# Optimization experiments

Measured on AMD Instinct MI355X. Metric: run time of the kernel, lower is better.

The kernel has to match this reference:

```python
import jax, jax.numpy as jnp
import numpy as np
from jax import lax

B, H, W = 8, 96, 160
CF = 64        # feature channels (= input_channels//2 = out_channels)
OC = 64        # out channels
K = 3          # kernel
G = 8          # deform (offset) groups
PAD, DIL = 1, 1


def conv3x3(x, w, b):
    y = lax.conv_general_dilated(x, w, (1, 1), ((PAD, PAD), (PAD, PAD)),
                                 dimension_numbers=('NCHW', 'OIHW', 'NCHW'))
    return y + b[None, :, None, None]


def lrelu(x):
    return jnp.where(x >= 0, x, 0.1 * x)


def deform_conv2d(x, offset, mask, w, b):
    # x: (B, Cin, H, W); offset: (B, 2*G*K*K, H, W) in (y, x) per tap; mask: (B, G*K*K, H, W)
    Bq, Cin, Hq, Wq = x.shape
    OCq = w.shape[0]
    off = offset.reshape(Bq, G, K, K, 2, Hq, Wq)
    dy, dx = off[:, :, :, :, 0], off[:, :, :, :, 1]        # (B,G,K,K,H,W)
    ky = jnp.arange(K, dtype=x.dtype).reshape(1, 1, K, 1, 1, 1)
    kx = jnp.arange(K, dtype=x.dtype).reshape(1, 1, 1, K, 1, 1)
    hy = jnp.arange(Hq, dtype=x.dtype).reshape(1, 1, 1, 1, Hq, 1)
    wx = jnp.arange(Wq, dtype=x.dtype).reshape(1, 1, 1, 1, 1, Wq)
    ys = dy + hy - PAD + ky * DIL                          # sampling rows
    xs = dx + wx - PAAD if False else dx + wx - PAD + kx * DIL  # sampling cols
    xg = x.reshape(Bq, G, Cin // G, Hq, Wq)

    def sample(img, ysg, xsg):
        # img: (Cg,H,W); ysg/xsg: (K,K,H,W) -> (Cg,K,K,H,W) bilinear with zero padding
        y0 = jnp.floor(ysg)
        x0 = jnp.floor(xsg)
        wy1 = ysg - y0
        wx1 = xsg - x0
        wy0 = 1.0 - wy1
        wx0 = 1.0 - wx1

        def gather(yi, xi):
            valid = ((yi >= 0) & (yi < Hq) & (xi >= 0) & (xi < Wq)).astype(img.dtype)
            yc = jnp.clip(yi, 0, Hq - 1).astype(jnp.int32)
            xc = jnp.clip(xi, 0, Wq - 1).astype(jnp.int32)
            return img[:, yc, xc] * valid[None]

        return (gather(y0, x0) * (wy0 * wx0)[None]
                + gather(y0, x0 + 1) * (wy0 * wx1)[None]
                + gather(y0 + 1, x0) * (wy1 * wx0)[None]
                + gather(y0 + 1, x0 + 1) * (wy1 * wx1)[None])

    sampled = jax.vmap(jax.vmap(sample))(xg, ys, xs)       # (B,G,Cg,K,K,H,W)
    sampled = sampled * mask.reshape(Bq, G, 1, K, K, Hq, Wq)
    wg = w.reshape(OCq, G, Cin // G, K, K)
    return jnp.einsum('bgcijhw,ogcij->bohw', sampled, wg) + b[None, :, None, None]


def setup_inputs() -> dict:
    key = jax.random.key(0)
    ks = jax.random.split(key, 12)
    cin0 = OC * 3 + 4  # 196

    def u(k, shape, fan_in):
        s = 1.0 / np.sqrt(fan_in)
        return jax.random.uniform(k, shape, jnp.float32, -s, s)

    inp = {
        'current_feature_warped': jax.random.normal(ks[0], (B, CF, H, W), jnp.float32),
        'feat_prop': jax.random.normal(ks[1], (B, CF, H, W), jnp.float32),
        'feat_prev': jax.random.normal(ks[2], (B, CF, H, W), jnp.float32),
        'flow1': jax.random.normal(ks[3], (B, 2, H, W), jnp.float32),
        'flow2': jax.random.normal(ks[4], (B, 2, H, W), jnp.float32),
        'w1': u(ks[5], (OC, cin0, 3, 3), cin0 * 9), 'b1': jnp.zeros((OC,), jnp.float32),
        'w2': u(ks[6], (OC, OC, 3, 3), OC * 9), 'b2': jnp.zeros((OC,), jnp.float32),
        'w3': u(ks[7], (OC, OC, 3, 3), OC * 9), 'b3': jnp.zeros((OC,), jnp.float32),
        'w4': u(ks[8], (K * K * 3 * G, OC, 3, 3), OC * 9), 'b4': jnp.zeros((K * K * 3 * G,), jnp.float32),
        'weight': u(ks[9], (OC, CF, 3, 3), 128 * 9),  # init_weights uses n = input_channels*k*k = 128*9
        'bias': jnp.zeros((OC,), jnp.float32),
    }
    return inp

# remove the accidental typo guard (keeps module exec-clean)
PAAD = PAD


def reference(current_feature_warped, feat_prop, feat_prev, flow1, flow2,
              w1, b1, w2, b2, w3, b3, w4, b4, weight, bias):
    cat = jnp.concatenate([current_feature_warped, feat_prop, feat_prev, flow1, flow2], axis=1)
    o = lrelu(conv3x3(cat, w1, b1))
    o = lrelu(conv3x3(o, w2, b2))
    o = lrelu(conv3x3(o, w3, b3))
    o = conv3x3(o, w4, b4)                                  # (B, 3*G*K*K, H, W)
    offset1, offset2, mask = jnp.split(o, 3, axis=1)        # each (B, G*K*K, H, W)
    rep = offset1.shape[1] // 2                             # G*K*K/2 = 36
    offset1 = offset1 + jnp.tile(flow1[:, ::-1], (1, rep, 1, 1))
    offset2 = offset2 + jnp.tile(flow2[:, ::-1], (1, rep, 1, 1))
    offset = jnp.concatenate([offset1, offset2], axis=1)    # (B, 2*G*K*K, H, W)
    mask = jax.nn.sigmoid(mask)
    return deform_conv2d(current_feature_warped, offset, mask, weight, bias)
```

## Files before the change

### kernel.cpp

```cpp
#include <hip/hip_runtime.h>
#include <hip/hip_bf16.h>
#include <math.h>

typedef __attribute__((ext_vector_type(8))) short short8;
typedef __attribute__((ext_vector_type(4))) float f32x4;

constexpr int B_ = 8, H_ = 96, W_ = 160;
constexpr int HW_ = H_ * W_;
constexpr int NPIX = B_ * HW_;

__device__ __forceinline__ unsigned short f2bf(float f) {
    unsigned int u = __builtin_bit_cast(unsigned int, f);
    u += 0x7FFFu + ((u >> 16) & 1u);
    return (unsigned short)(u >> 16);
}
__device__ __forceinline__ float bf2f(unsigned short s) {
    unsigned int u = ((unsigned int)s) << 16;
    return __builtin_bit_cast(float, u);
}
__device__ __forceinline__ unsigned int cvt_pk_bf16(float lo, float hi) {
    unsigned int r;
    asm volatile("v_cvt_pk_bf16_f32 %0, %1, %2" : "=v"(r) : "v"(lo), "v"(hi));
    return r;
}
__device__ __forceinline__ float f4get(const float4& v, int q) {
    switch (q) { case 0: return v.x; case 1: return v.y;
                 case 2: return v.z; default: return v.w; }
}

__global__ __launch_bounds__(256) void prep_x1(
    const float* __restrict__ cfw, const float* __restrict__ fpro,
    const float* __restrict__ fprv, const float* __restrict__ f1,
    const float* __restrict__ f2, unsigned short* __restrict__ X1)
{
    const int c8 = blockIdx.y;
    const int pix0 = blockIdx.x * 1024 + threadIdx.x * 4;
    unsigned short* dst = X1 + ((size_t)c8 * NPIX + pix0) * 8;

    if (c8 >= 25) {
        uint4 z = {0u, 0u, 0u, 0u};
        #pragma unroll
        for (int q = 0; q < 4; ++q) *(uint4*)(dst + q * 8) = z;
        return;
    }

    const int b  = pix0 / HW_;
    const int hw = pix0 - b * HW_;

    float4 v[8];
    #pragma unroll
    for (int j = 0; j < 8; ++j) {
        int c = c8 * 8 + j;
        const float* src = nullptr; int sc = 0, nc = 0;
        if (c < 64)       { src = cfw;  sc = c;       nc = 64; }
        else if (c < 128) { src = fpro; sc = c - 64;  nc = 64; }
        else if (c < 192) { src = fprv; sc = c - 128; nc = 64; }
        else if (c < 194) { src = f1;   sc = c - 192; nc = 2;  }
        else if (c < 196) { src = f2;   sc = c - 194; nc = 2;  }
        if (src) v[j] = *(const float4*)(src + ((size_t)b * nc + sc) * HW_ + hw);
        else     { v[j].x = v[j].y = v[j].z = v[j].w = 0.f; }
    }
    #pragma unroll
    for (int q = 0; q < 4; ++q) {
        uint4 o;
        o.x = cvt_pk_bf16(f4get(v[0], q), f4get(v[1], q));
        o.y = cvt_pk_bf16(f4get(v[2], q), f4get(v[3], q));
        o.z = cvt_pk_bf16(f4get(v[4], q), f4get(v[5], q));
        o.w = cvt_pk_bf16(f4get(v[6], q), f4get(v[7], q));
        *(uint4*)(dst + q * 8) = o;
    }
}

__device__ __forceinline__ void pack_conv_w(
    const float* __restrict__ w, unsigned short* __restrict__ Bt, int idx,
    int Cin, int KCH, int Nout, int NFTOT)
{
    int lane = idx & 63;
    int r = idx >> 6;
    int nf = r % NFTOT; r /= NFTOT;
    int ck = r % KCH;
    int t  = r / KCH;
    int n  = nf * 16 + (lane & 15);
    int kb = ck * 32 + (lane >> 4) * 8;
    short8 o;
    #pragma unroll
    for (int j = 0; j < 8; ++j) {
        int c = kb + j;
        float v = (c < Cin && n < Nout) ? w[((size_t)n * Cin + c) * 9 + t] : 0.f;
        o[j] = (short)f2bf(v);
    }
    *(short8*)(Bt + (size_t)idx * 8) = o;
}

__global__ __launch_bounds__(256) void prep_wall(
    const float* __restrict__ w1, const float* __restrict__ w2,
    const float* __restrict__ w3, const float* __restrict__ w4,
    const float* __restrict__ wd,
    unsigned short* __restrict__ Bt1, unsigned short* __restrict__ Bt2,
    unsigned short* __restrict__ Bt3, unsigned short* __restrict__ Bt4,
    unsigned short* __restrict__ Btd)
{
    int idx = blockIdx.x * 256 + threadIdx.x;
    if (idx < 16128)      pack_conv_w(w1, Bt1, idx,          196, 7,  64,  4);
    else if (idx < 20736) pack_conv_w(w2, Bt2, idx - 16128,   64, 2,  64,  4);
    else if (idx < 25344) pack_conv_w(w3, Bt3, idx - 20736,   64, 2,  64,  4);
    else if (idx < 41472) pack_conv_w(w4, Bt4, idx - 25344,   64, 2, 216, 14);
    else if (idx < 47616) {
        int id2 = idx - 41472;
        int lane = id2 & 63;
        int r = id2 >> 6;
        int nf = r % 4; r >>= 2;
        int ck = r % 3;
        int g  = r / 3;
        int n  = nf * 16 + (lane & 15);
        int kb = ck * 32 + (lane >> 4) * 8;
        short8 o;
        #pragma unroll
        for (int j = 0; j < 8; ++j) {
            int k = kb + j;
            int t = k >> 3, c = k & 7;
            float v = (t < 9) ? wd[((size_t)n * 64 + g * 8 + c) * 9 + t] : 0.f;
            o[j] = (short)f2bf(v);
        }
        *(short8*)(Btd + (size_t)id2 * 8) = o;
    }
}

template<int KCH, int NFTOT, int NF, bool RELU>
__global__ __launch_bounds__(256) void conv_mfma(
    const unsigned short* __restrict__ X, const unsigned short* __restrict__ Bt,
    const float* __restrict__ bias, unsigned short* __restrict__ Y,
    int CoutTot, int fBase0)
{
    static_assert(NF == 4, "staging assumes 4 KB step chunk");
    __shared__ __align__(16) unsigned short bsh[NF * 512];

    const int tid  = threadIdx.x;
    const int lane = tid & 63;
    const int wv   = tid >> 6;
    const int m0   = blockIdx.x * 128 + wv * 32;
    const int fBase = fBase0 + blockIdx.y * NF;
    const int lm = lane & 15;
    const int l16 = lane >> 4;

    int p[2], hh[2], wp[2];
    #pragma unroll
    for (int mf = 0; mf < 2; ++mf) {
        int pm = m0 + mf * 16 + lm;
        p[mf] = pm;
        hh[mf] = (pm / W_) % H_;
        wp[mf] = pm % W_;
    }

    f32x4 acc[2][NF];
    #pragma unroll
    for (int nf = 0; nf < NF; ++nf) {
        int oc = (fBase + nf) * 16 + lm;
        float bv = (oc < CoutTot) ? bias[oc] : 0.f;
        f32x4 a = {bv, bv, bv, bv};
        acc[0][nf] = a; acc[1][nf] = a;
    }

    const short8 zero = {0,0,0,0,0,0,0,0};
    constexpr int S = KCH * 9;

    uint4 bt = *(const uint4*)(Bt + (size_t)fBase * 512 + tid * 8);

    #pragma unroll
    for (int s = 0; s < S; ++s) {
        const int ck = s / 9, t = s % 9;
        __syncthreads();
        *(uint4*)(bsh + tid * 8) = bt;
        __syncthreads();
        if (s + 1 < S) {
            const int ck2 = (s + 1) / 9, t2 = (s + 1) % 9;
            bt = *(const uint4*)(Bt +
                ((size_t)(t2 * KCH + ck2) * NFTOT + fBase) * 512 + tid * 8);
        }
        const int di = t / 3 - 1, dj = t % 3 - 1;
        const unsigned short* Xp = X + (size_t)(ck * 4 + l16) * NPIX * 8;
        short8 bfr[NF];
        #pragma unroll
        for (int nf = 0; nf < NF; ++nf)
            bfr[nf] = *(const short8*)(bsh + nf * 512 + lane * 8);
        #pragma unroll
        for (int mf = 0; mf < 2; ++mf) {
            bool val = ((unsigned)(hh[mf] + di) < (unsigned)H_) &&
                       ((unsigned)(wp[mf] + dj) < (unsigned)W_);
            const unsigned short* ap = Xp + (size_t)(p[mf] + di * W_ + dj) * 8;
            short8 afr = val ? *(const short8*)ap : zero;
            #pragma unroll
            for (int nf = 0; nf < NF; ++nf)
                acc[mf][nf] = __builtin_amdgcn_mfma_f32_16x16x32_bf16(
                    afr, bfr[nf], acc[mf][nf], 0, 0, 0);
        }
    }

    const int prow = l16 * 4;
    #pragma unroll
    for (int mf = 0; mf < 2; ++mf)
        #pragma unroll
        for (int nf = 0; nf < NF; ++nf) {
            int oc = (fBase + nf) * 16 + lm;
            if (oc < CoutTot) {
                #pragma unroll
                for (int r = 0; r < 4; ++r) {
                    int pix = m0 + mf * 16 + prow + r;
                    float v = acc[mf][nf][r];
                    if (RELU) v = (v >= 0.f) ? v : 0.1f * v;
                    Y[((size_t)(oc >> 3) * NPIX + pix) * 8 + (oc & 7)] = f2bf(v);
                }
            }
        }
}

template<int HALF>
__global__ __launch_bounds__(256, 4) void conv4_mfma(
    const unsigned short* __restrict__ X, const unsigned short* __restrict__ Bt,
    const float* __restrict__ bias,
    unsigned short* __restrict__ oY, unsigned short* __restrict__ oX,
    unsigned short* __restrict__ oM)
{
    __shared__ __align__(16) unsigned short bsh[7 * 512];

    const int tid  = threadIdx.x;
    const int lane = tid & 63;
    const int wv   = tid >> 6;
    const int pix0 = blockIdx.x * 128;
    const int m0   = pix0 + wv * 32;
    const int lm = lane & 15;
    const int l16 = lane >> 4;
    constexpr int FB = HALF * 7;

    int p[2], hh[2], wp[2];
    #pragma unroll
    for (int mf = 0; mf < 2; ++mf) {
        int pm = m0 + mf * 16 + lm;
        p[mf] = pm;
        hh[mf] = (pm / W_) % H_;
        wp[mf] = pm % W_;
    }

    f32x4 acc[2][7];
    #pragma unroll
    for (int nf = 0; nf < 7; ++nf) {
        int oc = (FB + nf) * 16 + lm;
        float bv = (oc < 216) ? bias[oc] : 0.f;
        f32x4 a = {bv, bv, bv, bv};
        acc[0][nf] = a; acc[1][nf] = a;
    }

    const short8 zero = {0,0,0,0,0,0,0,0};
    const bool two = (tid < 192);

    uint4 bt0 = *(const uint4*)(Bt + (size_t)FB * 512 + tid * 8);
    uint4 bt1 = {0u, 0u, 0u, 0u};
    if (two) bt1 = *(const uint4*)(Bt + (size_t)FB * 512 + (256 + tid) * 8);

    #pragma unroll
    for (int s = 0; s < 18; ++s) {
        const int ck = s / 9, t = s % 9;
        __syncthreads();
        *(uint4*)(bsh + tid * 8) = bt0;
        if (two) *(uint4*)(bsh + (256 + tid) * 8) = bt1;
        __syncthreads();
        if (s + 1 < 18) {
            const int ck2 = (s + 1) / 9, t2 = (s + 1) % 9;
            const unsigned short* nb =
                Bt + ((size_t)((t2 * 2 + ck2) * 14 + FB)) * 512;
            bt0 = *(const uint4*)(nb + tid * 8);
            if (two) bt1 = *(const uint4*)(nb + (256 + tid) * 8);
        }
        const int di = t / 3 - 1, dj = t % 3 - 1;
        const unsigned short* Xp = X + (size_t)(ck * 4 + l16) * NPIX * 8;
        short8 afr[2];
        #pragma unroll
        for (int mf = 0; mf < 2; ++mf) {
            bool val = ((unsigned)(hh[mf] + di) < (unsigned)H_) &&
                       ((unsigned)(wp[mf] + dj) < (unsigned)W_);
            const unsigned short* ap = Xp + (size_t)(p[mf] + di * W_ + dj) * 8;
            afr[mf] = val ? *(const short8*)ap : zero;
        }
        #pragma unroll
        for (int nf = 0; nf < 7; ++nf) {
            short8 bfr = *(const short8*)(bsh + nf * 512 + lane * 8);
            acc[0][nf] = __builtin_amdgcn_mfma_f32_16x16x32_bf16(
                afr[0], bfr, acc[0][nf], 0, 0, 0);
            acc[1][nf] = __builtin_amdgcn_mfma_f32_16x16x32_bf16(
                afr[1], bfr, acc[1][nf], 0, 0, 0);
        }
    }

    const int prow = l16 * 4;
    #pragma unroll
    for (int mf = 0; mf < 2; ++mf) {
        const int pixb = m0 + mf * 16 + prow;
        #pragma unroll
        for (int nf = 0; nf < 7; ++nf) {
            const int nfg = FB + nf;
            const int oc = nfg * 16 + lm;
            if (nfg < 9) {
                const int pr = nfg * 8 + (lm >> 1);
                unsigned short* plane = ((lm & 1) ? oX : oY) + (size_t)pr * NPIX;
                uint2 sv;
                sv.x = cvt_pk_bf16(acc[mf][nf][0], acc[mf][nf][1]);
                sv.y = cvt_pk_bf16(acc[mf][nf][2], acc[mf][nf][3]);
                *(uint2*)(plane + pixb) = sv;
            } else if (oc < 216) {
                const int mi = (nfg - 9) * 16 + lm;
                float v0 = 1.f / (1.f + expf(-acc[mf][nf][0]));
                float v1 = 1.f / (1.f + expf(-acc[mf][nf][1]));
                float v2 = 1.f / (1.f + expf(-acc[mf][nf][2]));
                float v3 = 1.f / (1.f + expf(-acc[mf][nf][3]));
                uint2 sv;
                sv.x = cvt_pk_bf16(v0, v1);
                sv.y = cvt_pk_bf16(v2, v3);
                *(uint2*)(oM + (size_t)mi * NPIX + pixb) = sv;
            }
        }
    }
}

__global__ __launch_bounds__(128) void deform_mfma(
    const unsigned short* __restrict__ Xg,
    const unsigned short* __restrict__ oY,
    const unsigned short* __restrict__ oX,
    const unsigned short* __restrict__ oM,
    const float* __restrict__ f1, const float* __restrict__ f2,
    const unsigned short* __restrict__ Btd,
    const float* __restrict__ bia,
    float* __restrict__ out)
{
    __shared__ __align__(16) char lds[64 * 256];

    const int tid  = threadIdx.x;
    const int lane = tid & 63;
    const int wv   = tid >> 6;
    const int lm   = lane & 15;
    const int l16  = lane >> 4;
    const int pix0 = blockIdx.x * 64;
    const int b    = pix0 / HW_;
    const int hw0  = pix0 % HW_;

    const int pix = tid & 63;
    const int hi  = tid >> 6;
    const int hw  = hw0 + pix;
    const int h   = hw / W_;
    const int w   = hw - h * W_;
    const size_t gp = (size_t)(pix0 + pix);
    const size_t bF = (size_t)b * 2 * HW_;

    {
        uint4 z = {0u, 0u, 0u, 0u};
        #pragma unroll
        for (int i = 0; i < 8; ++i)
            ((uint4*)lds)[i * 128 + tid] = z;
    }

    f32x4 acc[2][4];
    #pragma unroll
    for (int nf = 0; nf < 4; ++nf) {
        float bv = bia[nf * 16 + lm];
        f32x4 a = {bv, bv, bv, bv};
        acc[0][nf] = a; acc[1][nf] = a;
    }

    for (int g = 0; g < 8; ++g) {
        const unsigned short* Xp = Xg + (size_t)g * NPIX * 8;
        __syncthreads();

        const float* fl = (g < 4) ? f1 : f2;
        const float fy = fl[bF + (size_t)HW_ + hw];
        const float fx = fl[bF + hw];
        unsigned short uy[5], ux[5], um[5];
        #pragma unroll
        for (int it = 0; it < 5; ++it) {
            int t = hi + 2 * it;
            bool act = (it < 4) || (hi == 0);
            if (act) {
                size_t po = (size_t)(g * 9 + t) * NPIX + gp;
                uy[it] = oY[po]; ux[it] = oX[po]; um[it] = oM[po];
            }
        }
        #pragma unroll
        for (int it = 0; it < 5; ++it) {
            int t = hi + 2 * it;
            bool act = (it < 4) || (hi == 0);
            if (act) {
                float dy = bf2f(uy[it]) + fy;
                float dx = bf2f(ux[it]) + fx;
                float m  = bf2f(um[it]);

                float ys = dy + (float)(h - 1 + t / 3);
                float xs = dx + (float)(w - 1 + t % 3);
                float y0f = floorf(ys), x0f = floorf(xs);
                float wy1 = ys - y0f, wx1 = xs - x0f;
                float wy0 = 1.f - wy1, wx0 = 1.f - wx1;
                int iy0 = (int)y0f, ix0 = (int)x0f;
                int iy1 = iy0 + 1,  ix1 = ix0 + 1;
                bool vy0 = (unsigned)iy0 < (unsigned)H_;
                bool vy1 = (unsigned)iy1 < (unsigned)H_;
                bool vx0 = (unsigned)ix0 < (unsigned)W_;
                bool vx1 = (unsigned)ix1 < (unsigned)W_;
                int cy0 = min(max(iy0, 0), H_ - 1), cy1 = min(max(iy1, 0), H_ - 1);
                int cx0 = min(max(ix0, 0), W_ - 1), cx1 = min(max(ix1, 0), W_ - 1);
                float w00 = (vy0 && vx0) ? wy0 * wx0 * m : 0.f;
                float w01 = (vy0 && vx1) ? wy0 * wx1 * m : 0.f;
                float w10 = (vy1 && vx0) ? wy1 * wx0 * m : 0.f;
                float w11 = (vy1 && vx1) ? wy1 * wx1 * m : 0.f;

                size_t r0 = (size_t)b * HW_ + (size_t)cy0 * W_;
                size_t r1 = (size_t)b * HW_ + (size_t)cy1 * W_;
                uint4 c00 = *(const uint4*)(Xp + (r0 + cx0) * 8);
                uint4 c01 = *(const uint4*)(Xp + (r0 + cx1) * 8);
                uint4 c10 = *(const uint4*)(Xp + (r1 + cx0) * 8);
                uint4 c11 = *(const uint4*)(Xp + (r1 + cx1) * 8);

                float a8[8];
                #pragma unroll
                for (int i = 0; i < 8; ++i) a8[i] = 0.f;
                const unsigned int u00[4] = {c00.x, c00.y, c00.z, c00.w};
                const unsigned int u01[4] = {c01.x, c01.y, c01.z, c01.w};
                const unsigned int u10[4] = {c10.x, c10.y, c10.z, c10.w};
                const unsigned int u11[4] = {c11.x, c11.y, c11.z, c11.w};
                #pragma unroll
                for (int i = 0; i < 4; ++i) {
                    a8[2*i]   += w00 * __builtin_bit_cast(float, u00[i] << 16);
                    a8[2*i+1] += w00 * __builtin_bit_cast(float, u00[i] & 0xFFFF0000u);
                    a8[2*i]   += w01 * __builtin_bit_cast(float, u01[i] << 16);
                    a8[2*i+1] += w01 * __builtin_bit_cast(float, u01[i] & 0xFFFF0000u);
                    a8[2*i]   += w10 * __builtin_bit_cast(float, u10[i] << 16);
                    a8[2*i+1] += w10 * __builtin_bit_cast(float, u10[i] & 0xFFFF0000u);
                    a8[2*i]   += w11 * __builtin_bit_cast(float, u11[i] << 16);
                    a8[2*i+1] += w11 * __builtin_bit_cast(float, u11[i] & 0xFFFF0000u);
                }
                uint4 ov;
                ov.x = cvt_pk_bf16(a8[0], a8[1]);
                ov.y = cvt_pk_bf16(a8[2], a8[3]);
                ov.z = cvt_pk_bf16(a8[4], a8[5]);
                ov.w = cvt_pk_bf16(a8[6], a8[7]);
                int slot = t ^ (pix & 7);
                *(uint4*)(lds + pix * 256 + slot * 16) = ov;
            }
        }
        __syncthreads();
        #pragma unroll
        for (int ck = 0; ck < 3; ++ck) {
            const short8* bpp = (const short8*)Btd + ((size_t)(g * 3 + ck) * 4) * 64 + lane;
            short8 bfr[4];
            #pragma unroll
            for (int nf = 0; nf < 4; ++nf) bfr[nf] = bpp[nf * 64];
            const int slotbase = ck * 4 + l16;
            #pragma unroll
            for (int mf = 0; mf < 2; ++mf) {
                int row = wv * 32 + mf * 16 + lm;
                int slot = slotbase ^ (lm & 7);
                short8 afr = *(const short8*)(lds + row * 256 + slot * 16);
                #pragma unroll
                for (int nf = 0; nf < 4; ++nf)
                    acc[mf][nf] = __builtin_amdgcn_mfma_f32_16x16x32_bf16(
                        afr, bfr[nf], acc[mf][nf], 0, 0, 0);
            }
        }
    }

    #pragma unroll
    for (int mf = 0; mf < 2; ++mf)
        #pragma unroll
        for (int nf = 0; nf < 4; ++nf) {
            int oc = nf * 16 + lm;
            int px = hw0 + wv * 32 + mf * 16 + l16 * 4;
            *(f32x4*)(out + (size_t)(b * 64 + oc) * HW_ + px) = acc[mf][nf];
        }
}

extern "C" void kernel_launch(void* const* d_in, const int* in_sizes, int n_in,
                              void* d_out, int out_size, void* d_ws, size_t ws_size,
                              hipStream_t stream)
{
    const float* cfw  = (const float*)d_in[0];
    const float* fpro = (const float*)d_in[1];
    const float* fprv = (const float*)d_in[2];
    const float* fl1  = (const float*)d_in[3];
    const float* fl2  = (const float*)d_in[4];
    const float* w1   = (const float*)d_in[5];
    const float* b1   = (const float*)d_in[6];
    const float* w2   = (const float*)d_in[7];
    const float* b2   = (const float*)d_in[8];
    const float* w3   = (const float*)d_in[9];
    const float* b3   = (const float*)d_in[10];
    const float* w4   = (const float*)d_in[11];
    const float* b4   = (const float*)d_in[12];
    const float* wdef = (const float*)d_in[13];
    const float* bdef = (const float*)d_in[14];
    float* out = (float*)d_out;

    char* ws = (char*)d_ws;
    unsigned short* X1  = (unsigned short*)(ws);
    unsigned short* buf1= (unsigned short*)(ws + 55050240);
    unsigned short* o2  = (unsigned short*)(ws + 70778880);
    unsigned short* oY  = (unsigned short*)(ws + 70778880);
    unsigned short* oX  = oY + (size_t)72 * NPIX;
    unsigned short* oM  = oX + (size_t)72 * NPIX;
    unsigned short* Bt1 = (unsigned short*)(ws + 125829120);
    unsigned short* Bt2 = (unsigned short*)(ws + 125829120 + 258048);
    unsigned short* Bt3 = (unsigned short*)(ws + 125829120 + 258048 + 73728);
    unsigned short* Bt4 = (unsigned short*)(ws + 125829120 + 258048 + 2*73728);
    unsigned short* Btd = (unsigned short*)(ws + 125829120 + 2*258048 + 2*73728);

    prep_x1<<<dim3(NPIX / 1024, 28), dim3(256), 0, stream>>>(
        cfw, fpro, fprv, fl1, fl2, X1);
    prep_wall<<<dim3((47616 + 255) / 256), dim3(256), 0, stream>>>(
        w1, w2, w3, w4, wdef, Bt1, Bt2, Bt3, Bt4, Btd);

    dim3 blk(256);
    dim3 gridM(NPIX / 128, 1);
    conv_mfma<7, 4, 4, true><<<gridM, blk, 0, stream>>>(X1, Bt1, b1, buf1, 64, 0);
    conv_mfma<2, 4, 4, true><<<gridM, blk, 0, stream>>>(buf1, Bt2, b2, o2, 64, 0);
    conv_mfma<2, 4, 4, true><<<gridM, blk, 0, stream>>>(o2, Bt3, b3, buf1, 64, 0);
    conv4_mfma<0><<<gridM, blk, 0, stream>>>(buf1, Bt4, b4, oY, oX, oM);
    conv4_mfma<1><<<gridM, blk, 0, stream>>>(buf1, Bt4, b4, oY, oX, oM);
    deform_mfma<<<dim3(NPIX / 64), dim3(128), 0, stream>>>(
        X1, oY, oX, oM, fl1, fl2, Btd, bdef, out);
}
```

Baseline: 253.0 us.

## Use four waves per block in deform kernel, splitting taps and output channels

The deformable-conv kernel goes from 128 to 256 threads per 64-pixel block. Bilinear sampling of the 9 taps is now spread over 4 waves (at most 3 taps per thread) instead of 2 (up to 5), which shortens the serial gather work per thread. In the MFMA stage each wave owns 16 output channels across all 64 pixels rather than 32 pixels across all 64 channels, so each wave holds one B fragment and 4 accumulators. The cost is more LDS A-fragment reads per wave and more idle threads on the ninth tap.

```diff
diff --git a/kernel.cpp b/kernel.cpp
--- a/kernel.cpp
+++ b/kernel.cpp
@@ -321,7 +321,7 @@
     }
 }
 
-__global__ __launch_bounds__(128) void deform_mfma(
+__global__ __launch_bounds__(256) void deform_mfma(
     const unsigned short* __restrict__ Xg,
     const unsigned short* __restrict__ oY,
     const unsigned short* __restrict__ oX,
@@ -343,7 +343,6 @@
     const int hw0  = pix0 % HW_;
 
     const int pix = tid & 63;
-    const int hi  = tid >> 6;
     const int hw  = hw0 + pix;
     const int h   = hw / W_;
     const int w   = hw - h * W_;
@@ -353,16 +352,16 @@
     {
         uint4 z = {0u, 0u, 0u, 0u};
         #pragma unroll
-        for (int i = 0; i < 8; ++i)
-            ((uint4*)lds)[i * 128 + tid] = z;
-    }
-
-    f32x4 acc[2][4];
-    #pragma unroll
-    for (int nf = 0; nf < 4; ++nf) {
-        float bv = bia[nf * 16 + lm];
+        for (int i = 0; i < 4; ++i)
+            ((uint4*)lds)[i * 256 + tid] = z;
+    }
+
+    f32x4 acc[4];
+    {
+        float bv = bia[wv * 16 + lm];
         f32x4 a = {bv, bv, bv, bv};
-        acc[0][nf] = a; acc[1][nf] = a;
+        #pragma unroll
+        for (int mf = 0; mf < 4; ++mf) acc[mf] = a;
     }
 
     for (int g = 0; g < 8; ++g) {
@@ -372,20 +371,20 @@
         const float* fl = (g < 4) ? f1 : f2;
         const float fy = fl[bF + (size_t)HW_ + hw];
         const float fx = fl[bF + hw];
-        unsigned short uy[5], ux[5], um[5];
-        #pragma unroll
-        for (int it = 0; it < 5; ++it) {
-            int t = hi + 2 * it;
-            bool act = (it < 4) || (hi == 0);
+        unsigned short uy[3], ux[3], um[3];
+        #pragma unroll
+        for (int it = 0; it < 3; ++it) {
+            int t = wv + 4 * it;
+            bool act = (it < 2) || (wv == 0);
             if (act) {
                 size_t po = (size_t)(g * 9 + t) * NPIX + gp;
                 uy[it] = oY[po]; ux[it] = oX[po]; um[it] = oM[po];
             }
         }
         #pragma unroll
-        for (int it = 0; it < 5; ++it) {
-            int t = hi + 2 * it;
-            bool act = (it < 4) || (hi == 0);
+        for (int it = 0; it < 3; ++it) {
+            int t = wv + 4 * it;
+            bool act = (it < 2) || (wv == 0);
             if (act) {
                 float dy = bf2f(uy[it]) + fy;
                 float dx = bf2f(ux[it]) + fx;
@@ -446,32 +445,25 @@
         __syncthreads();
         #pragma unroll
         for (int ck = 0; ck < 3; ++ck) {
-            const short8* bpp = (const short8*)Btd + ((size_t)(g * 3 + ck) * 4) * 64 + lane;
-            short8 bfr[4];
-            #pragma unroll
-            for (int nf = 0; nf < 4; ++nf) bfr[nf] = bpp[nf * 64];
+            short8 bfr = ((const short8*)Btd)[((size_t)(g * 3 + ck) * 4 + wv) * 64 + lane];
             const int slotbase = ck * 4 + l16;
             #pragma unroll
-            for (int mf = 0; mf < 2; ++mf) {
-                int row = wv * 32 + mf * 16 + lm;
+            for (int mf = 0; mf < 4; ++mf) {
+                int row = mf * 16 + lm;
                 int slot = slotbase ^ (lm & 7);
                 short8 afr = *(const short8*)(lds + row * 256 + slot * 16);
-                #pragma unroll
-                for (int nf = 0; nf < 4; ++nf)
-                    acc[mf][nf] = __builtin_amdgcn_mfma_f32_16x16x32_bf16(
-                        afr, bfr[nf], acc[mf][nf], 0, 0, 0);
+                acc[mf] = __builtin_amdgcn_mfma_f32_16x16x32_bf16(
+                    afr, bfr, acc[mf], 0, 0, 0);
             }
         }
     }
 
-    #pragma unroll
-    for (int mf = 0; mf < 2; ++mf)
-        #pragma unroll
-        for (int nf = 0; nf < 4; ++nf) {
-            int oc = nf * 16 + lm;
-            int px = hw0 + wv * 32 + mf * 16 + l16 * 4;
-            *(f32x4*)(out + (size_t)(b * 64 + oc) * HW_ + px) = acc[mf][nf];
-        }
+    const int oc = wv * 16 + lm;
+    #pragma unroll
+    for (int mf = 0; mf < 4; ++mf) {
+        int px = hw0 + mf * 16 + l16 * 4;
+        *(f32x4*)(out + (size_t)(b * 64 + oc) * HW_ + px) = acc[mf];
+    }
 }
 
 extern "C" void kernel_launch(void* const* d_in, const int* in_sizes, int n_in,
@@ -520,6 +512,6 @@
     conv_mfma<2, 4, 4, true><<<gridM, blk, 0, stream>>>(o2, Bt3, b3, buf1, 64, 0);
     conv4_mfma<0><<<gridM, blk, 0, stream>>>(buf1, Bt4, b4, oY, oX, oM);
     conv4_mfma<1><<<gridM, blk, 0, stream>>>(buf1, Bt4, b4, oY, oX, oM);
-    deform_mfma<<<dim3(NPIX / 64), dim3(128), 0, stream>>>(
+    deform_mfma<<<dim3(NPIX / 64), blk, 0, stream>>>(
         X1, oY, oX, oM, fl1, fl2, Btd, bdef, out);
 }
```

Result: no change. 252.3 us (-0.3%).
